# Kernel tuning notes

Hardware: AMD Instinct MI355X
Metric: run time of the kernel (lower is better)

Reference implementation:

```python
import jax, jax.numpy as jnp
import numpy as np


def setup_inputs() -> dict:
    key = jax.random.key(0)
    k1, k2 = jax.random.split(key, 2)
    B, K, N, Fdim = 32, 8, 2048, 64
    regime_probs = jax.random.uniform(k1, (B, K), dtype=jnp.float32)
    factor_loadings = jax.random.normal(k2, (K, N, Fdim), dtype=jnp.float32)
    specific_risk = jnp.ones((K, N), dtype=jnp.float32)
    return {
        "regime_probs": regime_probs,
        "factor_loadings": factor_loadings,
        "specific_risk": specific_risk,
    }


def reference(regime_probs, factor_loadings, specific_risk):
    # Handle [B, K, T] -> take last time step (as in original)
    if regime_probs.ndim == 3:
        regime_probs = regime_probs[:, :, -1]
    K, N, _ = factor_loadings.shape
    # Per-regime covariance: F_k F_k^T + diag(specific_risk_k^2)  -> [K, N, N]
    cov_k = jnp.einsum("knf,kmf->knm", factor_loadings, factor_loadings)
    eye = jnp.eye(N, dtype=cov_k.dtype)
    cov_k = cov_k + eye[None, :, :] * (specific_risk ** 2)[:, :, None]
    # Regime-weighted mixture per batch element -> [B, N, N]
    return jnp.einsum("bk,knm->bnm", regime_probs, cov_k)
```

## Files before the change

### kernel.cpp

```cpp
#include <hip/hip_runtime.h>

#define NDIM 2048
#define FDIM 64
#define KDIM 8
#define BDIM 32
#define TILE 64
#define BFROW 72
#define FROW  68

typedef __attribute__((ext_vector_type(8))) short short8;
typedef __attribute__((ext_vector_type(4))) float f32x4;

static __device__ __forceinline__ unsigned short f2bf(float x) {
    unsigned u = __float_as_uint(x);
    return (unsigned short)((u + 0x7fffu + ((u >> 16) & 1u)) >> 16);
}

__global__ __launch_bounds__(256, 2) void rfm_fused_mfma(
    const float* __restrict__ p, const float* __restrict__ L,
    const float* __restrict__ sr, float* __restrict__ out)
{
    __shared__ float pl[BDIM * KDIM];
    __shared__ __align__(16) char smem[2 * TILE * FROW * 4];

    unsigned short* An = (unsigned short*)smem;
    unsigned short* Am = An + TILE * BFROW;
    float* Pn = (float*)smem;
    float* Pm = Pn + TILE * FROW;

    const int n0 = blockIdx.y * TILE;
    const int m0 = blockIdx.x * TILE;
    const int t  = threadIdx.x;
    const int lane = t & 63;
    const int w   = t >> 6;
    const int wr  = w >> 1;
    const int wc  = w & 1;
    const int l15 = lane & 15;
    const int l4  = lane >> 4;

    pl[t] = p[t];

    f32x4 acc[KDIM][2][2];
    #pragma unroll
    for (int k = 0; k < KDIM; ++k)
        #pragma unroll
        for (int ti = 0; ti < 2; ++ti)
            #pragma unroll
            for (int tj = 0; tj < 2; ++tj)
                acc[k][ti][tj] = (f32x4){0.f, 0.f, 0.f, 0.f};

    #pragma unroll
    for (int k = 0; k < KDIM; ++k) {
        const float* Lk = L + (size_t)k * (NDIM * FDIM);

        #pragma unroll
        for (int r = 0; r < 4; ++r) {
            const int idx = t + r * 256;
            const int row = idx >> 4;
            const int fc  = (idx & 15) << 2;
            const float4 va = *(const float4*)&Lk[(size_t)(n0 + row) * FDIM + fc];
            const float4 vb = *(const float4*)&Lk[(size_t)(m0 + row) * FDIM + fc];
            ushort4 ua, ub;
            ua.x = f2bf(va.x); ua.y = f2bf(va.y); ua.z = f2bf(va.z); ua.w = f2bf(va.w);
            ub.x = f2bf(vb.x); ub.y = f2bf(vb.y); ub.z = f2bf(vb.z); ub.w = f2bf(vb.w);
            *(ushort4*)&An[row * BFROW + fc] = ua;
            *(ushort4*)&Am[row * BFROW + fc] = ub;
        }
        __syncthreads();

        short8 af[2][2], bv[2][2];
        #pragma unroll
        for (int ti = 0; ti < 2; ++ti)
            #pragma unroll
            for (int s = 0; s < 2; ++s) {
                af[ti][s] = *(const short8*)
                    &An[(wr * 32 + ti * 16 + l15) * BFROW + s * 32 + l4 * 8];
                bv[ti][s] = *(const short8*)
                    &Am[(wc * 32 + ti * 16 + l15) * BFROW + s * 32 + l4 * 8];
            }
        #pragma unroll
        for (int ti = 0; ti < 2; ++ti)
            #pragma unroll
            for (int tj = 0; tj < 2; ++tj)
                #pragma unroll
                for (int s = 0; s < 2; ++s)
                    acc[k][ti][tj] = __builtin_amdgcn_mfma_f32_16x16x32_bf16(
                        af[ti][s], bv[tj][s], acc[k][ti][tj], 0, 0, 0);
        __syncthreads();
    }

    if (n0 == m0 && wr == wc) {
        #pragma unroll
        for (int k = 0; k < KDIM; ++k)
            #pragma unroll
            for (int ti = 0; ti < 2; ++ti)
                #pragma unroll
                for (int reg = 0; reg < 4; ++reg) {
                    const int row = l4 * 4 + reg;
                    if (row == l15) {
                        const float q = sr[k * NDIM + n0 + wr * 32 + ti * 16 + row];
                        acc[k][ti][ti][reg] += q * q;
                    }
                }
    }

    const size_t NN = (size_t)NDIM * NDIM;
    const int tx = t & 15;
    const int ty = t >> 4;
    float* obase = out + (size_t)n0 * NDIM + m0;

    #pragma unroll 1
    for (int b = 0; b < BDIM; b += 2) {
        float pa[KDIM], pb[KDIM];
        #pragma unroll
        for (int k = 0; k < KDIM; ++k) {
            pa[k] = pl[b * KDIM + k];
            pb[k] = pl[(b + 1) * KDIM + k];
        }
        #pragma unroll
        for (int ti = 0; ti < 2; ++ti)
            #pragma unroll
            for (int tj = 0; tj < 2; ++tj)
                #pragma unroll
                for (int reg = 0; reg < 4; ++reg) {
                    const int rl = wr * 32 + ti * 16 + l4 * 4 + reg;
                    const int cl = wc * 32 + tj * 16 + l15;
                    float va = 0.f, vb = 0.f;
                    #pragma unroll
                    for (int k = 0; k < KDIM; ++k) {
                        va += pa[k] * acc[k][ti][tj][reg];
                        vb += pb[k] * acc[k][ti][tj][reg];
                    }
                    Pn[rl * FROW + cl] = va;
                    Pm[rl * FROW + cl] = vb;
                }
        __syncthreads();
        #pragma unroll
        for (int q = 0; q < 4; ++q) {
            const int row = ty + 16 * q;
            const f32x4 wa = *(const f32x4*)&Pn[row * FROW + tx * 4];
            const f32x4 wb = *(const f32x4*)&Pm[row * FROW + tx * 4];
            float* dst = obase + (size_t)row * NDIM + tx * 4;
            *(f32x4*)(dst + (size_t)b * NN)       = wa;
            *(f32x4*)(dst + (size_t)(b + 1) * NN) = wb;
        }
        __syncthreads();
    }
}

extern "C" void kernel_launch(void* const* d_in, const int* in_sizes, int n_in,
                              void* d_out, int out_size, void* d_ws, size_t ws_size,
                              hipStream_t stream)
{
    const float* p  = (const float*)d_in[0];
    const float* L  = (const float*)d_in[1];
    const float* sr = (const float*)d_in[2];
    float* out = (float*)d_out;

    dim3 grid(NDIM / TILE, NDIM / TILE);
    hipLaunchKernelGGL(rfm_fused_mfma, grid, dim3(256), 0, stream,
                       p, L, sr, out);
}
```

Measured before the change: 134.2 us.

## Double-buffer loading-tile staging and epilogue mixing buffers to cut barriers

Two ping-pong schemes are added. The GEMM phase now stages the next regime's bf16 loading tiles into a second LDS buffer while MFMAs run on the current one. The epilogue alternates between two pairs of LDS output buffers, so the mixing for the next batch pair overlaps the global stores of the current pair, and it uses one raw barrier per step instead of two __syncthreads. The cost is twice the LDS footprint (about 68KB per block), which may limit occupancy. The kernel remains dominated by its large output writes.

```diff
diff --git a/kernel.cpp b/kernel.cpp
--- a/kernel.cpp
+++ b/kernel.cpp
@@ -21,12 +21,16 @@
     const float* __restrict__ sr, float* __restrict__ out)
 {
     __shared__ float pl[BDIM * KDIM];
-    __shared__ __align__(16) char smem[2 * TILE * FROW * 4];
+    __shared__ __align__(16) char smem[4 * TILE * FROW * 4];
 
-    unsigned short* An = (unsigned short*)smem;
-    unsigned short* Am = An + TILE * BFROW;
-    float* Pn = (float*)smem;
-    float* Pm = Pn + TILE * FROW;
+    unsigned short* const An0 = (unsigned short*)smem;
+    unsigned short* const Am0 = An0 + TILE * BFROW;
+    unsigned short* const An1 = Am0 + TILE * BFROW;
+    unsigned short* const Am1 = An1 + TILE * BFROW;
+    float* const P0 = (float*)smem;
+    float* const P1 = (float*)(smem + 1 * TILE * FROW * 4);
+    float* const P2 = (float*)(smem + 2 * TILE * FROW * 4);
+    float* const P3 = (float*)(smem + 3 * TILE * FROW * 4);
 
     const int n0 = blockIdx.y * TILE;
     const int m0 = blockIdx.x * TILE;
@@ -40,19 +44,8 @@
 
     pl[t] = p[t];
 
-    f32x4 acc[KDIM][2][2];
-    #pragma unroll
-    for (int k = 0; k < KDIM; ++k)
-        #pragma unroll
-        for (int ti = 0; ti < 2; ++ti)
-            #pragma unroll
-            for (int tj = 0; tj < 2; ++tj)
-                acc[k][ti][tj] = (f32x4){0.f, 0.f, 0.f, 0.f};
-
-    #pragma unroll
-    for (int k = 0; k < KDIM; ++k) {
+    auto STAGE = [&](int k, unsigned short* A, unsigned short* B) {
         const float* Lk = L + (size_t)k * (NDIM * FDIM);
-
         #pragma unroll
         for (int r = 0; r < 4; ++r) {
             const int idx = t + r * 256;
@@ -63,20 +56,38 @@
             ushort4 ua, ub;
             ua.x = f2bf(va.x); ua.y = f2bf(va.y); ua.z = f2bf(va.z); ua.w = f2bf(va.w);
             ub.x = f2bf(vb.x); ub.y = f2bf(vb.y); ub.z = f2bf(vb.z); ub.w = f2bf(vb.w);
-            *(ushort4*)&An[row * BFROW + fc] = ua;
-            *(ushort4*)&Am[row * BFROW + fc] = ub;
+            *(ushort4*)&A[row * BFROW + fc] = ua;
+            *(ushort4*)&B[row * BFROW + fc] = ub;
         }
-        __syncthreads();
+    };
 
+    f32x4 acc[KDIM][2][2];
+    #pragma unroll
+    for (int k = 0; k < KDIM; ++k)
+        #pragma unroll
+        for (int ti = 0; ti < 2; ++ti)
+            #pragma unroll
+            for (int tj = 0; tj < 2; ++tj)
+                acc[k][ti][tj] = (f32x4){0.f, 0.f, 0.f, 0.f};
+
+    STAGE(0, An0, Am0);
+    __syncthreads();
+    #pragma unroll
+    for (int k = 0; k < KDIM; ++k) {
+        if (k + 1 < KDIM)
+            STAGE(k + 1, (k & 1) ? An0 : An1, (k & 1) ? Am0 : Am1);
+
+        const unsigned short* Ac = (k & 1) ? An1 : An0;
+        const unsigned short* Bc = (k & 1) ? Am1 : Am0;
         short8 af[2][2], bv[2][2];
         #pragma unroll
         for (int ti = 0; ti < 2; ++ti)
             #pragma unroll
             for (int s = 0; s < 2; ++s) {
                 af[ti][s] = *(const short8*)
-                    &An[(wr * 32 + ti * 16 + l15) * BFROW + s * 32 + l4 * 8];
+                    &Ac[(wr * 32 + ti * 16 + l15) * BFROW + s * 32 + l4 * 8];
                 bv[ti][s] = *(const short8*)
-                    &Am[(wc * 32 + ti * 16 + l15) * BFROW + s * 32 + l4 * 8];
+                    &Bc[(wc * 32 + ti * 16 + l15) * BFROW + s * 32 + l4 * 8];
             }
         #pragma unroll
         for (int ti = 0; ti < 2; ++ti)
@@ -104,18 +115,17 @@
                 }
     }
 
-    const size_t NN = (size_t)NDIM * NDIM;
     const int tx = t & 15;
     const int ty = t >> 4;
+    const size_t NN = (size_t)NDIM * NDIM;
     float* obase = out + (size_t)n0 * NDIM + m0;
 
-    #pragma unroll 1
-    for (int b = 0; b < BDIM; b += 2) {
+    auto MIX2 = [&](int b0, float* Qa, float* Qb) {
         float pa[KDIM], pb[KDIM];
         #pragma unroll
         for (int k = 0; k < KDIM; ++k) {
-            pa[k] = pl[b * KDIM + k];
-            pb[k] = pl[(b + 1) * KDIM + k];
+            pa[k] = pl[b0 * KDIM + k];
+            pb[k] = pl[(b0 + 1) * KDIM + k];
         }
         #pragma unroll
         for (int ti = 0; ti < 2; ++ti)
@@ -125,26 +135,44 @@
                 for (int reg = 0; reg < 4; ++reg) {
                     const int rl = wr * 32 + ti * 16 + l4 * 4 + reg;
                     const int cl = wc * 32 + tj * 16 + l15;
-                    float va = 0.f, vb = 0.f;
+                    float va = 0.0f, vb = 0.0f;
                     #pragma unroll
                     for (int k = 0; k < KDIM; ++k) {
                         va += pa[k] * acc[k][ti][tj][reg];
                         vb += pb[k] * acc[k][ti][tj][reg];
                     }
-                    Pn[rl * FROW + cl] = va;
-                    Pm[rl * FROW + cl] = vb;
+                    Qa[rl * FROW + cl] = va;
+                    Qb[rl * FROW + cl] = vb;
                 }
-        __syncthreads();
+    };
+    auto STORE2 = [&](int b0, const float* Qa, const float* Qb) {
         #pragma unroll
         for (int q = 0; q < 4; ++q) {
             const int row = ty + 16 * q;
-            const f32x4 wa = *(const f32x4*)&Pn[row * FROW + tx * 4];
-            const f32x4 wb = *(const f32x4*)&Pm[row * FROW + tx * 4];
-            float* dst = obase + (size_t)row * NDIM + tx * 4;
-            *(f32x4*)(dst + (size_t)b * NN)       = wa;
-            *(f32x4*)(dst + (size_t)(b + 1) * NN) = wb;
+            const f32x4 wa = *(const f32x4*)&Qa[row * FROW + tx * 4];
+            const f32x4 wb = *(const f32x4*)&Qb[row * FROW + tx * 4];
+            *(f32x4*)(obase + (size_t)b0 * NN
+                            + (size_t)row * NDIM + tx * 4) = wa;
+            *(f32x4*)(obase + (size_t)(b0 + 1) * NN
+                            + (size_t)row * NDIM + tx * 4) = wb;
         }
-        __syncthreads();
+    };
+    auto BAR = [&]() {
+        asm volatile("s_waitcnt lgkmcnt(0)" ::: "memory");
+        __builtin_amdgcn_s_barrier();
+        __builtin_amdgcn_sched_barrier(0);
+    };
+
+    MIX2(0, P0, P1);
+    BAR();
+    #pragma unroll 1
+    for (int pp = 0; pp < 16; pp += 2) {
+        MIX2(2 * (pp + 1), P2, P3);
+        STORE2(2 * pp, P0, P1);
+        BAR();
+        if (pp + 2 < 16) MIX2(2 * (pp + 2), P0, P1);
+        STORE2(2 * (pp + 1), P2, P3);
+        BAR();
     }
 }
 
```

After: 126.8 us. 1.06x faster.

## Swap MFMA operands to store output directly from registers, dropping LDS staging

Applied to the files above, without the earlier changes.

Swaps the MFMA A/B operands so each lane's four accumulator values are contiguous along the output row. The epilogue can then write float4 stores straight from registers. This removes the shared-memory transpose buffer and the two barriers per batch pair in the epilogue, and shrinks LDS use. In exchange, each store instruction now covers only 16-byte segments spread over 16 rows, which is less coalesced than the previous staged full-row writes.

```diff
diff --git a/kernel.cpp b/kernel.cpp
--- a/kernel.cpp
+++ b/kernel.cpp
@@ -6,7 +6,6 @@
 #define BDIM 32
 #define TILE 64
 #define BFROW 72
-#define FROW  68
 
 typedef __attribute__((ext_vector_type(8))) short short8;
 typedef __attribute__((ext_vector_type(4))) float f32x4;
@@ -21,12 +20,8 @@
     const float* __restrict__ sr, float* __restrict__ out)
 {
     __shared__ float pl[BDIM * KDIM];
-    __shared__ __align__(16) char smem[2 * TILE * FROW * 4];
-
-    unsigned short* An = (unsigned short*)smem;
-    unsigned short* Am = An + TILE * BFROW;
-    float* Pn = (float*)smem;
-    float* Pm = Pn + TILE * FROW;
+    __shared__ __align__(16) unsigned short An[TILE][BFROW];
+    __shared__ __align__(16) unsigned short Am[TILE][BFROW];
 
     const int n0 = blockIdx.y * TILE;
     const int m0 = blockIdx.x * TILE;
@@ -44,10 +39,10 @@
     #pragma unroll
     for (int k = 0; k < KDIM; ++k)
         #pragma unroll
-        for (int ti = 0; ti < 2; ++ti)
+        for (int tm = 0; tm < 2; ++tm)
             #pragma unroll
-            for (int tj = 0; tj < 2; ++tj)
-                acc[k][ti][tj] = (f32x4){0.f, 0.f, 0.f, 0.f};
+            for (int tn = 0; tn < 2; ++tn)
+                acc[k][tm][tn] = (f32x4){0.f, 0.f, 0.f, 0.f};
 
     #pragma unroll
     for (int k = 0; k < KDIM; ++k) {
@@ -63,8 +58,8 @@
             ushort4 ua, ub;
             ua.x = f2bf(va.x); ua.y = f2bf(va.y); ua.z = f2bf(va.z); ua.w = f2bf(va.w);
             ub.x = f2bf(vb.x); ub.y = f2bf(vb.y); ub.z = f2bf(vb.z); ub.w = f2bf(vb.w);
-            *(ushort4*)&An[row * BFROW + fc] = ua;
-            *(ushort4*)&Am[row * BFROW + fc] = ub;
+            *(ushort4*)&An[row][fc] = ua;
+            *(ushort4*)&Am[row][fc] = ub;
         }
         __syncthreads();
 
@@ -74,77 +69,70 @@
             #pragma unroll
             for (int s = 0; s < 2; ++s) {
                 af[ti][s] = *(const short8*)
-                    &An[(wr * 32 + ti * 16 + l15) * BFROW + s * 32 + l4 * 8];
+                    &An[wr * 32 + ti * 16 + l15][s * 32 + l4 * 8];
                 bv[ti][s] = *(const short8*)
-                    &Am[(wc * 32 + ti * 16 + l15) * BFROW + s * 32 + l4 * 8];
+                    &Am[wc * 32 + ti * 16 + l15][s * 32 + l4 * 8];
             }
         #pragma unroll
-        for (int ti = 0; ti < 2; ++ti)
+        for (int tm = 0; tm < 2; ++tm)
             #pragma unroll
-            for (int tj = 0; tj < 2; ++tj)
+            for (int tn = 0; tn < 2; ++tn)
                 #pragma unroll
                 for (int s = 0; s < 2; ++s)
-                    acc[k][ti][tj] = __builtin_amdgcn_mfma_f32_16x16x32_bf16(
-                        af[ti][s], bv[tj][s], acc[k][ti][tj], 0, 0, 0);
+                    acc[k][tm][tn] = __builtin_amdgcn_mfma_f32_16x16x32_bf16(
+                        bv[tm][s], af[tn][s], acc[k][tm][tn], 0, 0, 0);
         __syncthreads();
     }
 
-    if (n0 == m0 && wr == wc) {
+    #pragma unroll
+    for (int tm = 0; tm < 2; ++tm)
         #pragma unroll
-        for (int k = 0; k < KDIM; ++k)
+        for (int tn = 0; tn < 2; ++tn)
             #pragma unroll
-            for (int ti = 0; ti < 2; ++ti)
-                #pragma unroll
-                for (int reg = 0; reg < 4; ++reg) {
-                    const int row = l4 * 4 + reg;
-                    if (row == l15) {
-                        const float q = sr[k * NDIM + n0 + wr * 32 + ti * 16 + row];
-                        acc[k][ti][ti][reg] += q * q;
+            for (int reg = 0; reg < 4; ++reg) {
+                const int gn = n0 + wr * 32 + tn * 16 + l15;
+                const int gm = m0 + wc * 32 + tm * 16 + l4 * 4 + reg;
+                if (gn == gm) {
+                    #pragma unroll
+                    for (int k = 0; k < KDIM; ++k) {
+                        const float q = sr[k * NDIM + gn];
+                        acc[k][tm][tn][reg] += q * q;
                     }
                 }
-    }
+            }
 
     const size_t NN = (size_t)NDIM * NDIM;
-    const int tx = t & 15;
-    const int ty = t >> 4;
-    float* obase = out + (size_t)n0 * NDIM + m0;
+    float* optr[2][2];
+    #pragma unroll
+    for (int tm = 0; tm < 2; ++tm)
+        #pragma unroll
+        for (int tn = 0; tn < 2; ++tn)
+            optr[tm][tn] = out
+                + (size_t)(n0 + wr * 32 + tn * 16 + l15) * NDIM
+                + (m0 + wc * 32 + tm * 16 + l4 * 4);
 
     #pragma unroll 1
-    for (int b = 0; b < BDIM; b += 2) {
-        float pa[KDIM], pb[KDIM];
+    for (int b = 0; b < BDIM; ++b) {
+        float pb[KDIM];
         #pragma unroll
-        for (int k = 0; k < KDIM; ++k) {
-            pa[k] = pl[b * KDIM + k];
-            pb[k] = pl[(b + 1) * KDIM + k];
-        }
+        for (int k = 0; k < KDIM; ++k) pb[k] = pl[b * KDIM + k];
+        const size_t boff = (size_t)b * NN;
         #pragma unroll
-        for (int ti = 0; ti < 2; ++ti)
+        for (int tm = 0; tm < 2; ++tm)
             #pragma unroll
-            for (int tj = 0; tj < 2; ++tj)
+            for (int tn = 0; tn < 2; ++tn) {
+                float v0 = 0.f, v1 = 0.f, v2 = 0.f, v3 = 0.f;
                 #pragma unroll
-                for (int reg = 0; reg < 4; ++reg) {
-                    const int rl = wr * 32 + ti * 16 + l4 * 4 + reg;
-                    const int cl = wc * 32 + tj * 16 + l15;
-                    float va = 0.f, vb = 0.f;
-                    #pragma unroll
-                    for (int k = 0; k < KDIM; ++k) {
-                        va += pa[k] * acc[k][ti][tj][reg];
-                        vb += pb[k] * acc[k][ti][tj][reg];
-                    }
-                    Pn[rl * FROW + cl] = va;
-                    Pm[rl * FROW + cl] = vb;
+                for (int k = 0; k < KDIM; ++k) {
+                    v0 += pb[k] * acc[k][tm][tn][0];
+                    v1 += pb[k] * acc[k][tm][tn][1];
+                    v2 += pb[k] * acc[k][tm][tn][2];
+                    v3 += pb[k] * acc[k][tm][tn][3];
                 }
-        __syncthreads();
-        #pragma unroll
-        for (int q = 0; q < 4; ++q) {
-            const int row = ty + 16 * q;
-            const f32x4 wa = *(const f32x4*)&Pn[row * FROW + tx * 4];
-            const f32x4 wb = *(const f32x4*)&Pm[row * FROW + tx * 4];
-            float* dst = obase + (size_t)row * NDIM + tx * 4;
-            *(f32x4*)(dst + (size_t)b * NN)       = wa;
-            *(f32x4*)(dst + (size_t)(b + 1) * NN) = wb;
-        }
-        __syncthreads();
+                f32x4 r;
+                r[0] = v0; r[1] = v1; r[2] = v2; r[3] = v3;
+                *(f32x4*)(optr[tm][tn] + boff) = r;
+            }
     }
 }
 
```

Result: slower. 143.8 us (+7.2%).

## Exploit covariance symmetry: compute upper-triangular tiles and write transposed mirrors

Applied to the files above, without the earlier changes.

The 2D tile grid becomes a 1D grid of 528 blocks covering only diagonal and upper-triangular 64x64 tiles. Each off-diagonal block also writes its transpose through extra LDS staging buffers, which roughly halves the MFMA and L-load work. Output writes switch to nontemporal stores, and the __syncthreads calls become explicit lgkmcnt waits plus barriers. The kernel stays bound by writing the 512MB output, so the gain may be limited, and the doubled LDS (about 70KB) could cut occupancy.

```diff
diff --git a/kernel.cpp b/kernel.cpp
--- a/kernel.cpp
+++ b/kernel.cpp
@@ -21,15 +21,27 @@
     const float* __restrict__ sr, float* __restrict__ out)
 {
     __shared__ float pl[BDIM * KDIM];
-    __shared__ __align__(16) char smem[2 * TILE * FROW * 4];
+    __shared__ __align__(16) char smem[4 * TILE * FROW * 4];
 
-    unsigned short* An = (unsigned short*)smem;
-    unsigned short* Am = An + TILE * BFROW;
-    float* Pn = (float*)smem;
-    float* Pm = Pn + TILE * FROW;
+    unsigned short* const An = (unsigned short*)smem;
+    unsigned short* const Am = An + TILE * BFROW;
+    float* const P0 = (float*)smem;
+    float* const T0 = P0 + TILE * FROW;
+    float* const P1 = T0 + TILE * FROW;
+    float* const T1 = P1 + TILE * FROW;
 
-    const int n0 = blockIdx.y * TILE;
-    const int m0 = blockIdx.x * TILE;
+    const int id = blockIdx.x;
+    int r, c;
+    if (id < 32) { r = id; c = id; }
+    else {
+        int i = id - 32, rr = 0;
+        while (i >= 31 - rr) { i -= 31 - rr; ++rr; }
+        r = rr; c = rr + 1 + i;
+    }
+    const int n0 = r * TILE;
+    const int m0 = c * TILE;
+    const bool diag = (r == c);
+
     const int t  = threadIdx.x;
     const int lane = t & 63;
     const int w   = t >> 6;
@@ -54,8 +66,8 @@
         const float* Lk = L + (size_t)k * (NDIM * FDIM);
 
         #pragma unroll
-        for (int r = 0; r < 4; ++r) {
-            const int idx = t + r * 256;
+        for (int rq = 0; rq < 4; ++rq) {
+            const int idx = t + rq * 256;
             const int row = idx >> 4;
             const int fc  = (idx & 15) << 2;
             const float4 va = *(const float4*)&Lk[(size_t)(n0 + row) * FDIM + fc];
@@ -89,7 +101,7 @@
         __syncthreads();
     }
 
-    if (n0 == m0 && wr == wc) {
+    if (diag && wr == wc) {
         #pragma unroll
         for (int k = 0; k < KDIM; ++k)
             #pragma unroll
@@ -107,7 +119,6 @@
     const size_t NN = (size_t)NDIM * NDIM;
     const int tx = t & 15;
     const int ty = t >> 4;
-    float* obase = out + (size_t)n0 * NDIM + m0;
 
     #pragma unroll 1
     for (int b = 0; b < BDIM; b += 2) {
@@ -125,26 +136,46 @@
                 for (int reg = 0; reg < 4; ++reg) {
                     const int rl = wr * 32 + ti * 16 + l4 * 4 + reg;
                     const int cl = wc * 32 + tj * 16 + l15;
-                    float va = 0.f, vb = 0.f;
+                    float va = 0.0f, vb = 0.0f;
                     #pragma unroll
                     for (int k = 0; k < KDIM; ++k) {
                         va += pa[k] * acc[k][ti][tj][reg];
                         vb += pb[k] * acc[k][ti][tj][reg];
                     }
-                    Pn[rl * FROW + cl] = va;
-                    Pm[rl * FROW + cl] = vb;
+                    P0[rl * FROW + cl] = va;
+                    P1[rl * FROW + cl] = vb;
+                    if (!diag) {
+                        T0[cl * FROW + rl] = va;
+                        T1[cl * FROW + rl] = vb;
+                    }
                 }
-        __syncthreads();
+        asm volatile("s_waitcnt lgkmcnt(0)" ::: "memory");
+        __builtin_amdgcn_s_barrier();
+        __builtin_amdgcn_sched_barrier(0);
+
         #pragma unroll
         for (int q = 0; q < 4; ++q) {
             const int row = ty + 16 * q;
-            const f32x4 wa = *(const f32x4*)&Pn[row * FROW + tx * 4];
-            const f32x4 wb = *(const f32x4*)&Pm[row * FROW + tx * 4];
-            float* dst = obase + (size_t)row * NDIM + tx * 4;
-            *(f32x4*)(dst + (size_t)b * NN)       = wa;
-            *(f32x4*)(dst + (size_t)(b + 1) * NN) = wb;
+            const f32x4 wa = *(const f32x4*)&P0[row * FROW + tx * 4];
+            const f32x4 wb = *(const f32x4*)&P1[row * FROW + tx * 4];
+            float* dst = out + (size_t)(n0 + row) * NDIM + m0 + tx * 4;
+            __builtin_nontemporal_store(wa, (f32x4*)(dst + (size_t)b * NN));
+            __builtin_nontemporal_store(wb, (f32x4*)(dst + (size_t)(b + 1) * NN));
         }
-        __syncthreads();
+        if (!diag) {
+            #pragma unroll
+            for (int q = 0; q < 4; ++q) {
+                const int row = ty + 16 * q;
+                const f32x4 wa = *(const f32x4*)&T0[row * FROW + tx * 4];
+                const f32x4 wb = *(const f32x4*)&T1[row * FROW + tx * 4];
+                float* dst = out + (size_t)(m0 + row) * NDIM + n0 + tx * 4;
+                __builtin_nontemporal_store(wa, (f32x4*)(dst + (size_t)b * NN));
+                __builtin_nontemporal_store(wb, (f32x4*)(dst + (size_t)(b + 1) * NN));
+            }
+        }
+        asm volatile("s_waitcnt lgkmcnt(0)" ::: "memory");
+        __builtin_amdgcn_s_barrier();
+        __builtin_amdgcn_sched_barrier(0);
     }
 }
 
@@ -157,7 +188,6 @@
     const float* sr = (const float*)d_in[2];
     float* out = (float*)d_out;
 
-    dim3 grid(NDIM / TILE, NDIM / TILE);
-    hipLaunchKernelGGL(rfm_fused_mfma, grid, dim3(256), 0, stream,
+    hipLaunchKernelGGL(rfm_fused_mfma, dim3(528), dim3(256), 0, stream,
                        p, L, sr, out);
 }
```

New measurement: 136.5 us. About the same (+1.7%).
